# Kernel optimization log

Hardware: AMD Instinct MI355X
Metric: run time of the kernel (lower is better)

## Reference

```python
import jax, jax.numpy as jnp
import numpy as np

TOPK = 20
TEMP = 1.0
B, N = 256, 50000


def _idcg_vector(topk):
    # idcg_vector[k-1] = sum_{i=0}^{k-1} 1/log2(i+2)
    return jnp.cumsum(1.0 / jnp.log2(jnp.arange(topk, dtype=jnp.float32) + 2.0))


def setup_inputs() -> dict:
    key = jax.random.key(0)
    k1, k2, k3 = jax.random.split(key, 3)
    scores_top = jax.random.normal(k1, (B, TOPK), dtype=jnp.float32)
    scores = jax.random.normal(k2, (B, N), dtype=jnp.float32)
    labels = jax.random.randint(k3, (B, TOPK), 0, 2).astype(jnp.float32)
    return {"scores_top": scores_top, "scores": scores, "labels": labels}


def reference(scores_top, scores, labels):
    # SmoothRank: rank_j = sum_i sigmoid((scores_i - scores_top_j)/temp) + 0.5
    diff = (scores[:, None, :] - scores_top[:, :, None]) / TEMP  # (B, topk, N)
    ranks = jnp.sum(jax.nn.sigmoid(diff), axis=-1) + 0.5          # (B, topk)
    d = jnp.log2(ranks + 1.0)
    dg = labels / d                                               # (B, topk)
    # dcg@p for p=1..topk is a cumulative sum (replaces the Python loop)
    dcg = jnp.cumsum(dg, axis=-1)                                 # (B, topk)
    idcg = _idcg_vector(TOPK)
    k_sum = jnp.sum(labels, axis=-1).astype(jnp.int32)            # (B,)
    p = jnp.arange(1, TOPK + 1, dtype=jnp.int32)                  # (topk,)
    k_clamped = jnp.minimum(k_sum[:, None], p[None, :])           # (B, topk)
    ndcg = dcg / idcg[k_clamped - 1]
    return ndcg
```

## Files before the change

kernel.cpp:

```cpp
#include <hip/hip_runtime.h>

#define TOPK 20
#define NITEMS 50000
#define BLOCK 1024
#define NBINS 2048
#define CHUNKS 32
#define STEPS 64
#define XMAX 6.0f
#define SCALE (2048.0f / 12.0f)
#define DELTA (12.0f / 2048.0f)
#define RSCALE (12.0f / 2048.0f / 4096.0f)
#define KSTRIDE 0.8290291182f

__global__ __launch_bounds__(BLOCK) void smoothdcg_kernel(
    const float* __restrict__ scores_top,
    const float* __restrict__ scores,
    const float* __restrict__ labels,
    float* __restrict__ out)
{
    const int b   = blockIdx.x;
    const int tid = threadIdx.x;

    __shared__ unsigned int hist[NBINS];
    __shared__ float s_t[TOPK];
    __shared__ float s_rank[TOPK];

#pragma unroll
    for (int i = tid; i < NBINS; i += BLOCK) hist[i] = 0u;
    if (tid < TOPK) s_t[tid] = scores_top[b * TOPK + tid];
    __syncthreads();

    const float4* row = (const float4*)(scores + (size_t)b * NITEMS);
    const int n4 = NITEMS / 4;

    float4 v = make_float4(0.f, 0.f, 0.f, 0.f);
    if (tid < n4) v = row[tid];

    for (int i = tid; i < n4; i += BLOCK) {
        const int inext = i + BLOCK;
        float4 vn = v;
        if (inext < n4) vn = row[inext];

        float s4[4] = {v.x, v.y, v.z, v.w};
#pragma unroll
        for (int k = 0; k < 4; ++k) {
            float s = fminf(fmaxf(s4[k], -5.9999f), 5.9999f);
            float f = fmaf(s, SCALE, 1024.0f);
            int idx  = (int)f;
            float ff = f - (float)idx;
            unsigned int contrib = (unsigned int)fmaf(ff, 4096.0f, 1048576.0f);
            atomicAdd(&hist[idx], contrib);
        }
        v = vn;
    }
    __syncthreads();

    if (tid < TOPK * CHUNKS) {
        const int j  = tid >> 5;
        const int qc = tid & 31;
        const float t  = s_t[j];
        const float x0 = fmaf((float)qc + 0.5f, DELTA, -XMAX);
        float u = __expf(t - x0);
        float accW = 0.0f;
        float accQ = 0.0f;
        int m = qc;
#pragma unroll 8
        for (int p = 0; p < STEPS; ++p) {
            unsigned int word = hist[m];
            unsigned int w  = word >> 20;
            int Q = (int)(word & 0xFFFFFu) - (int)(w << 11);
            float wf = (float)w;
            float Qf = (float)Q;
            float sg  = __builtin_amdgcn_rcpf(1.0f + u);
            float sgp = fmaf(-sg, sg, sg);
            accW = fmaf(wf, sg, accW);
            accQ = fmaf(Qf, sgp, accQ);
            u *= KSTRIDE;
            m += CHUNKS;
        }
        float acc = fmaf(accQ, RSCALE, accW);
#pragma unroll
        for (int off = 16; off >= 1; off >>= 1)
            acc += __shfl_down(acc, off, 64);
        if ((tid & 31) == 0) s_rank[j] = acc;
    }
    __syncthreads();

    if (tid == 0) {
        float idcg[TOPK];
        float run = 0.0f;
        for (int i = 0; i < TOPK; ++i) {
            run += 1.0f / log2f((float)i + 2.0f);
            idcg[i] = run;
        }
        float lab[TOPK];
        int ksum = 0;
        for (int j = 0; j < TOPK; ++j) {
            lab[j] = labels[b * TOPK + j];
            ksum += (int)(lab[j] + 0.5f);
        }
        float dcg = 0.0f;
        for (int j = 0; j < TOPK; ++j) {
            float rank = s_rank[j] + 0.5f;
            float d = log2f(rank + 1.0f);
            dcg += lab[j] / d;
            int kc  = (ksum < (j + 1)) ? ksum : (j + 1);
            int idx = kc - 1;
            if (idx < 0) idx += TOPK;
            out[b * TOPK + j] = dcg / idcg[idx];
        }
    }
}

extern "C" void kernel_launch(void* const* d_in, const int* in_sizes, int n_in,
                              void* d_out, int out_size, void* d_ws, size_t ws_size,
                              hipStream_t stream) {
    const float* scores_top = (const float*)d_in[0];
    const float* scores     = (const float*)d_in[1];
    const float* labels     = (const float*)d_in[2];
    float* out              = (float*)d_out;

    const int B = in_sizes[0] / TOPK;
    smoothdcg_kernel<<<dim3(B), dim3(BLOCK), 0, stream>>>(scores_top, scores, labels, out);
}
```

Baseline: 93.91 us.

## Split each row across two blocks with partial-rank merge via atomic counter

```diff
diff --git a/kernel.cpp b/kernel.cpp
--- a/kernel.cpp
+++ b/kernel.cpp
@@ -2,46 +2,55 @@
 
 #define TOPK 20
 #define NITEMS 50000
-#define BLOCK 1024
+#define BLOCK 512
+#define SPLIT 2
+#define HALF_N (NITEMS / SPLIT)
+#define NH4 (HALF_N / 4)
 #define NBINS 2048
-#define CHUNKS 32
-#define STEPS 64
+#define CHUNKS 16
+#define STEPS (NBINS / CHUNKS)
 #define XMAX 6.0f
 #define SCALE (2048.0f / 12.0f)
 #define DELTA (12.0f / 2048.0f)
 #define RSCALE (12.0f / 2048.0f / 4096.0f)
-#define KSTRIDE 0.8290291182f
+#define KSTRIDE 0.9105103651f
+#define PSTRIDE 32
 
 __global__ __launch_bounds__(BLOCK) void smoothdcg_kernel(
     const float* __restrict__ scores_top,
     const float* __restrict__ scores,
     const float* __restrict__ labels,
-    float* __restrict__ out)
+    float* __restrict__ out,
+    float* __restrict__ partials,
+    unsigned int* __restrict__ counters)
 {
-    const int b   = blockIdx.x;
-    const int tid = threadIdx.x;
+    const int bid  = blockIdx.x;
+    const int row  = bid >> 1;
+    const int half = bid & 1;
+    const int tid  = threadIdx.x;
 
     __shared__ unsigned int hist[NBINS];
     __shared__ float s_t[TOPK];
-    __shared__ float s_rank[TOPK];
+    __shared__ int   s_finish;
 
 #pragma unroll
     for (int i = tid; i < NBINS; i += BLOCK) hist[i] = 0u;
-    if (tid < TOPK) s_t[tid] = scores_top[b * TOPK + tid];
+    if (tid < TOPK) s_t[tid] = scores_top[row * TOPK + tid];
     __syncthreads();
 
-    const float4* row = (const float4*)(scores + (size_t)b * NITEMS);
-    const int n4 = NITEMS / 4;
+    const float4* rp = (const float4*)(scores + (size_t)row * NITEMS + (size_t)half * HALF_N);
 
-    float4 v = make_float4(0.f, 0.f, 0.f, 0.f);
-    if (tid < n4) v = row[tid];
+    float4 v0 = make_float4(0.f, 0.f, 0.f, 0.f);
+    float4 v1 = v0;
+    if (tid < NH4)         v0 = rp[tid];
+    if (tid + BLOCK < NH4) v1 = rp[tid + BLOCK];
 
-    for (int i = tid; i < n4; i += BLOCK) {
-        const int inext = i + BLOCK;
-        float4 vn = v;
-        if (inext < n4) vn = row[inext];
+    for (int i = tid; i < NH4; i += BLOCK) {
+        float4 v2 = v1;
+        const int i2 = i + 2 * BLOCK;
+        if (i2 < NH4) v2 = rp[i2];
 
-        float s4[4] = {v.x, v.y, v.z, v.w};
+        float s4[4] = {v0.x, v0.y, v0.z, v0.w};
 #pragma unroll
         for (int k = 0; k < 4; ++k) {
             float s = fminf(fmaxf(s4[k], -5.9999f), 5.9999f);
@@ -51,63 +60,76 @@
             unsigned int contrib = (unsigned int)fmaf(ff, 4096.0f, 1048576.0f);
             atomicAdd(&hist[idx], contrib);
         }
-        v = vn;
+        v0 = v1; v1 = v2;
     }
     __syncthreads();
 
     if (tid < TOPK * CHUNKS) {
-        const int j  = tid >> 5;
-        const int qc = tid & 31;
+        const int j  = tid >> 4;
+        const int qc = tid & 15;
         const float t  = s_t[j];
         const float x0 = fmaf((float)qc + 0.5f, DELTA, -XMAX);
         float u = __expf(t - x0);
-        float accW = 0.0f;
-        float accQ = 0.0f;
+        float accW = 0.0f, accQ = 0.0f;
         int m = qc;
 #pragma unroll 8
         for (int p = 0; p < STEPS; ++p) {
             unsigned int word = hist[m];
             unsigned int w  = word >> 20;
             int Q = (int)(word & 0xFFFFFu) - (int)(w << 11);
-            float wf = (float)w;
-            float Qf = (float)Q;
             float sg  = __builtin_amdgcn_rcpf(1.0f + u);
             float sgp = fmaf(-sg, sg, sg);
-            accW = fmaf(wf, sg, accW);
-            accQ = fmaf(Qf, sgp, accQ);
+            accW = fmaf((float)w, sg, accW);
+            accQ = fmaf((float)Q, sgp, accQ);
             u *= KSTRIDE;
             m += CHUNKS;
         }
         float acc = fmaf(accQ, RSCALE, accW);
 #pragma unroll
-        for (int off = 16; off >= 1; off >>= 1)
+        for (int off = 8; off >= 1; off >>= 1)
             acc += __shfl_down(acc, off, 64);
-        if ((tid & 31) == 0) s_rank[j] = acc;
+        if (qc == 0) partials[bid * PSTRIDE + j] = acc;
+    }
+
+    __syncthreads();
+    if (tid == 0) {
+        __threadfence();
+        unsigned int old = atomicAdd(&counters[row], 1u);
+        s_finish = (old == 1);
+        if (old == 1) __threadfence();
     }
     __syncthreads();
 
-    if (tid == 0) {
-        float idcg[TOPK];
-        float run = 0.0f;
-        for (int i = 0; i < TOPK; ++i) {
-            run += 1.0f / log2f((float)i + 2.0f);
-            idcg[i] = run;
+    if (s_finish && tid < 64) {
+        const int lane = tid;
+        float p = 0.0f, lab = 0.0f;
+        if (lane < TOPK) {
+            p = partials[(2 * row) * PSTRIDE + lane]
+              + partials[(2 * row + 1) * PSTRIDE + lane];
+            lab = labels[row * TOPK + lane];
         }
-        float lab[TOPK];
-        int ksum = 0;
-        for (int j = 0; j < TOPK; ++j) {
-            lab[j] = labels[b * TOPK + j];
-            ksum += (int)(lab[j] + 0.5f);
+        float rank = p + 0.5f;
+        float d  = __log2f(rank + 1.0f);
+        float dg = (lane < TOPK) ? lab / d : 0.0f;
+#pragma unroll
+        for (int off = 1; off < 32; off <<= 1) {
+            float tmp = __shfl_up(dg, off, 64);
+            if (lane >= off) dg += tmp;
         }
-        float dcg = 0.0f;
-        for (int j = 0; j < TOPK; ++j) {
-            float rank = s_rank[j] + 0.5f;
-            float d = log2f(rank + 1.0f);
-            dcg += lab[j] / d;
-            int kc  = (ksum < (j + 1)) ? ksum : (j + 1);
+        unsigned long long mk = __ballot(lab > 0.5f);
+        int ksum = __popcll(mk & 0xFFFFFull);
+        float r = (lane < TOPK) ? 1.0f / __log2f((float)lane + 2.0f) : 0.0f;
+#pragma unroll
+        for (int off = 1; off < 32; off <<= 1) {
+            float tmp = __shfl_up(r, off, 64);
+            if (lane >= off) r += tmp;
+        }
+        if (lane < TOPK) {
+            int kc  = (ksum < lane + 1) ? ksum : (lane + 1);
             int idx = kc - 1;
             if (idx < 0) idx += TOPK;
-            out[b * TOPK + j] = dcg / idcg[idx];
+            float iv = __shfl(r, idx, 64);
+            out[row * TOPK + lane] = dg / iv;
         }
     }
 }
@@ -121,5 +143,10 @@
     float* out              = (float*)d_out;
 
     const int B = in_sizes[0] / TOPK;
-    smoothdcg_kernel<<<dim3(B), dim3(BLOCK), 0, stream>>>(scores_top, scores, labels, out);
+    float* partials        = (float*)d_ws;
+    unsigned int* counters = (unsigned int*)((char*)d_ws + 65536);
+
+    hipMemsetAsync(counters, 0, B * sizeof(unsigned int), stream);
+    smoothdcg_kernel<<<dim3(B * SPLIT), dim3(BLOCK), 0, stream>>>(
+        scores_top, scores, labels, out, partials, counters);
 }
```

Result: slower. 107.0 us (+13.9%).
